# Kernel optimization log

Measured on AMD Instinct MI355X. Metric: run time of the kernel, lower is better.

Reference implementation:

```python
import jax, jax.numpy as jnp
import numpy as np

N_NODES = 100000
N_EDGES = 3200000
IN_C = 256
HID = 32
OUT_C = 64


def setup_inputs() -> dict:
    key = jax.random.key(0)
    ks = jax.random.split(key, 12)
    x = jax.random.normal(ks[0], (N_NODES, IN_C), dtype=jnp.float32)
    edge_index = jax.random.randint(ks[1], (2, N_EDGES), 0, N_NODES, dtype=jnp.int64)

    def lin(kw, kb, fan_in, fan_out):
        bound = 1.0 / np.sqrt(fan_in)
        W = jax.random.uniform(kw, (fan_out, fan_in), jnp.float32, -bound, bound)
        b = jax.random.uniform(kb, (fan_out,), jnp.float32, -bound, bound)
        return W, b

    W0, b0 = lin(ks[2], ks[3], IN_C, HID)
    W1, b1 = lin(ks[4], ks[5], HID, HID)
    W2, b2 = lin(ks[6], ks[7], HID, HID)
    W3, b3 = lin(ks[8], ks[9], HID, HID)
    W4, b4 = lin(ks[10], ks[11], HID, OUT_C)
    return {"x": x, "edge_index": edge_index,
            "W0": W0, "b0": b0, "W1": W1, "b1": b1, "W2": W2, "b2": b2,
            "W3": W3, "b3": b3, "W4": W4, "b4": b4}


def _gcn_norm(edge_index, num_nodes):
    # add self loops, symmetric normalization (PyG gcn_norm, edge_weight = 1)
    loop = jnp.arange(num_nodes, dtype=edge_index.dtype)
    row = jnp.concatenate([edge_index[0], loop])  # source nodes
    col = jnp.concatenate([edge_index[1], loop])  # target nodes
    deg = jax.ops.segment_sum(jnp.ones_like(col, dtype=jnp.float32), col,
                              num_segments=num_nodes)
    dinv = jnp.where(deg > 0, jax.lax.rsqrt(jnp.maximum(deg, 1e-12)), 0.0)
    norm = dinv[row] * dinv[col]
    return row, col, norm


def reference(x, edge_index, W0, b0, W1, b1, W2, b2, W3, b3, W4, b4):
    row, col, norm = _gcn_norm(edge_index, N_NODES)

    def prop(h):
        # gather source features, scale by norm, scatter-add to targets
        return jax.ops.segment_sum(norm[:, None] * h[row], col,
                                   num_segments=N_NODES)

    def sgconv(h, W, b):  # SGConv with K=1: propagate then linear
        return prop(h) @ W.T + b

    h = x @ W0.T + b0
    h = jax.nn.relu(sgconv(h, W1, b1))
    h = jax.nn.relu(sgconv(h, W2, b2))
    h = jax.nn.relu(sgconv(h, W3, b3))
    return h @ W4.T + b4
```

## Files before the change

### kernel.cpp

```cpp
#include <hip/hip_runtime.h>
#include <hip/hip_fp16.h>

#define N_NODES 100000
#define N_EDGES 3200000
#define IN_C 256
#define HID 32
#define OUT_C 64
#define CAP 80
#define NP 100032
#define BINW 256
#define BSH 8
#define NBIN 391
#define BCHUNK 8192

__device__ __forceinline__ float dot4(const float4 a, const float4 b) {
    return a.x * b.x + a.y * b.y + a.z * b.z + a.w * b.w;
}

__device__ __forceinline__ float4 h4tof4(uint2 v) {
    __half2 a = *reinterpret_cast<__half2*>(&v.x);
    __half2 b = *reinterpret_cast<__half2*>(&v.y);
    float2 fa = __half22float2(a), fb = __half22float2(b);
    return make_float4(fa.x, fa.y, fb.x, fb.y);
}
__device__ __forceinline__ uint2 f4toh4(float4 f) {
    __half2 a = __float22half2_rn(make_float2(f.x, f.y));
    __half2 b = __float22half2_rn(make_float2(f.z, f.w));
    uint2 v;
    v.x = *reinterpret_cast<unsigned int*>(&a);
    v.y = *reinterpret_cast<unsigned int*>(&b);
    return v;
}


__global__ __launch_bounds__(256) void k_binhist(const int* __restrict__ col,
                                                 int* __restrict__ binCnt) {
    __shared__ int h[NBIN];
    const int t = threadIdx.x;
    for (int i = t; i < NBIN; i += 256) h[i] = 0;
    __syncthreads();
    const long e0 = (long)blockIdx.x * BCHUNK;
    const long e1 = min((long)N_EDGES, e0 + BCHUNK);
    for (long i = e0 + t; i < e1; i += 256)
        atomicAdd(&h[col[i] >> BSH], 1);
    __syncthreads();
    for (int i = t; i < NBIN; i += 256)
        if (h[i]) atomicAdd(&binCnt[i], h[i]);
}

__global__ void k_binscan(const int* __restrict__ binCnt,
                          int* __restrict__ binStart, int* __restrict__ binCursor) {
    __shared__ int buf[2][512];
    const int t = threadIdx.x;
    int v = (t < NBIN) ? binCnt[t] : 0;
    buf[0][t] = v;
    __syncthreads();
    int s = 0;
    for (int off = 1; off < 512; off <<= 1) {
        int d = s ^ 1;
        int val = buf[s][t];
        if (t >= off) val += buf[s][t - off];
        buf[d][t] = val;
        __syncthreads();
        s = d;
    }
    if (t < NBIN) {
        int st = buf[s][t] - v;
        binStart[t] = st;
        binCursor[t] = st;
    }
}

__global__ __launch_bounds__(256) void k_binscatter(const int* __restrict__ row,
                                                    const int* __restrict__ col,
                                                    int* __restrict__ binCursor,
                                                    int2* __restrict__ pairs) {
    __shared__ int cnt[NBIN];
    __shared__ int ofs[NBIN];
    const int t = threadIdx.x;
    for (int i = t; i < NBIN; i += 256) cnt[i] = 0;
    __syncthreads();
    const long e0 = (long)blockIdx.x * BCHUNK;
    const long e1 = min((long)N_EDGES, e0 + BCHUNK);
    for (long i = e0 + t; i < e1; i += 256)
        atomicAdd(&cnt[col[i] >> BSH], 1);
    __syncthreads();
    for (int i = t; i < NBIN; i += 256) {
        int c = cnt[i];
        ofs[i] = c ? atomicAdd(&binCursor[i], c) : 0;
        cnt[i] = 0;
    }
    __syncthreads();
    for (long i = e0 + t; i < e1; i += 256) {
        int c = col[i];
        int b = c >> BSH;
        int p = ofs[b] + atomicAdd(&cnt[b], 1);
        pairs[p] = make_int2(row[i], c);
    }
}

__global__ __launch_bounds__(256) void k_binbuild(const int2* __restrict__ pairs,
                                                  const int* __restrict__ binStart,
                                                  const int* __restrict__ binCnt,
                                                  int* __restrict__ bucket,
                                                  int* __restrict__ degc,
                                                  float* __restrict__ dinv) {
    __shared__ int cur[BINW];
    const int t = threadIdx.x;
    const int bin = blockIdx.x;
    const int base = bin * BINW;
    cur[t] = 0;
    __syncthreads();
    const int s = binStart[bin], cn = binCnt[bin];
    for (int i = t; i < cn; i += 256) {
        int2 e = pairs[s + i];
        int c = e.y - base;
        int pos = atomicAdd(&cur[c], 1);
        if (pos < CAP) bucket[(size_t)(base + c) * CAP + pos] = e.x;
    }
    __syncthreads();
    int n = base + t;
    if (n < N_NODES) {
        int d = cur[t];
        degc[n] = d;
        dinv[n] = 1.0f / sqrtf((float)(d + 1));
    }
}


__global__ void k_hist(const int* __restrict__ col, int* __restrict__ deg) {
    int i = blockIdx.x * 256 + threadIdx.x;
    if (i < N_EDGES) atomicAdd(&deg[col[i]], 1);
}

__global__ void k_scan1(const int* __restrict__ deg, int* __restrict__ rowptr,
                        int* __restrict__ bsum) {
    __shared__ int buf[2][1024];
    const int t = threadIdx.x, b = blockIdx.x;
    const int i = b * 1024 + t;
    int v = (i < N_NODES) ? deg[i] : 0;
    buf[0][t] = v;
    __syncthreads();
    int src = 0;
    for (int off = 1; off < 1024; off <<= 1) {
        int dst = src ^ 1;
        int val = buf[src][t];
        if (t >= off) val += buf[src][t - off];
        buf[dst][t] = val;
        __syncthreads();
        src = dst;
    }
    int incl = buf[src][t];
    if (i < N_NODES) rowptr[i] = incl - v;
    if (t == 1023) bsum[b] = incl;
}

__global__ void k_scan2(int* __restrict__ bsum, int nb) {
    __shared__ int buf[2][128];
    const int t = threadIdx.x;
    int v = (t < nb) ? bsum[t] : 0;
    buf[0][t] = v;
    __syncthreads();
    int src = 0;
    for (int off = 1; off < 128; off <<= 1) {
        int dst = src ^ 1;
        int val = buf[src][t];
        if (t >= off) val += buf[src][t - off];
        buf[dst][t] = val;
        __syncthreads();
        src = dst;
    }
    if (t < nb) bsum[t] = buf[src][t] - v;
}

__global__ void k_scan3(int* __restrict__ rowptr, const int* __restrict__ bsum) {
    int i = blockIdx.x * 256 + threadIdx.x;
    if (i < N_NODES) rowptr[i] += bsum[i >> 10];
}

__global__ void k_dinv(const int* __restrict__ cnt, int stride,
                       float* __restrict__ dinv, int* __restrict__ degc) {
    int i = blockIdx.x * 256 + threadIdx.x;
    if (i < N_NODES) {
        int d = cnt[i * stride];
        degc[i] = d;
        dinv[i] = 1.0f / sqrtf((float)(d + 1));
    }
}

__global__ void k_scatter(const int* __restrict__ row, const int* __restrict__ col,
                          const int* __restrict__ rowptr, int* __restrict__ cursor,
                          int* __restrict__ csr) {
    int i = blockIdx.x * 256 + threadIdx.x;
    if (i < N_EDGES) {
        int c = col[i];
        int pos = rowptr[c] + atomicAdd(&cursor[c], 1);
        csr[pos] = row[i];
    }
}

__global__ __launch_bounds__(256) void k_lin0(const float4* __restrict__ x4,
                                              const float4* __restrict__ W04,
                                              const float4* __restrict__ b04,
                                              const float* __restrict__ dinv,
                                              uint2* __restrict__ g2) {
    __shared__ float4 Ws[2048];
    const int t = threadIdx.x;
    #pragma unroll
    for (int j = 0; j < 8; ++j) Ws[t + 256 * j] = W04[t + 256 * j];
    __syncthreads();

    const int l = t & 7;
    const int n0 = blockIdx.x * 64 + (t >> 3) * 2;
    if (n0 >= N_NODES) return;
    const bool two = (n0 + 1 < N_NODES);

    float a0[32], a1[32];
    #pragma unroll
    for (int c = 0; c < 32; ++c) { a0[c] = 0.f; a1[c] = 0.f; }

    const float4* xr0 = x4 + (size_t)n0 * 64;
    const float4* xr1 = xr0 + (two ? 64 : 0);
    #pragma unroll
    for (int kk = 0; kk < 8; ++kk) {
        float4 v0 = xr0[kk * 8 + l];
        float4 v1 = xr1[kk * 8 + l];
        #pragma unroll
        for (int c = 0; c < 32; ++c) {
            float4 w = Ws[c * 64 + kk * 8 + l];
            a0[c] += dot4(w, v0);
            a1[c] += dot4(w, v1);
        }
    }
    #pragma unroll
    for (int c = 0; c < 16; ++c) {
        float p0 = a0[c] + __shfl_xor(a0[c], 4, 8);
        float q0 = a0[c + 16] + __shfl_xor(a0[c + 16], 4, 8);
        a0[c] = (l & 4) ? q0 : p0;
        float p1 = a1[c] + __shfl_xor(a1[c], 4, 8);
        float q1 = a1[c + 16] + __shfl_xor(a1[c + 16], 4, 8);
        a1[c] = (l & 4) ? q1 : p1;
    }
    #pragma unroll
    for (int c = 0; c < 8; ++c) {
        float p0 = a0[c] + __shfl_xor(a0[c], 2, 8);
        float q0 = a0[c + 8] + __shfl_xor(a0[c + 8], 2, 8);
        a0[c] = (l & 2) ? q0 : p0;
        float p1 = a1[c] + __shfl_xor(a1[c], 2, 8);
        float q1 = a1[c + 8] + __shfl_xor(a1[c + 8], 2, 8);
        a1[c] = (l & 2) ? q1 : p1;
    }
    #pragma unroll
    for (int c = 0; c < 4; ++c) {
        float p0 = a0[c] + __shfl_xor(a0[c], 1, 8);
        float q0 = a0[c + 4] + __shfl_xor(a0[c + 4], 1, 8);
        a0[c] = (l & 1) ? q0 : p0;
        float p1 = a1[c] + __shfl_xor(a1[c], 1, 8);
        float q1 = a1[c + 4] + __shfl_xor(a1[c + 4], 1, 8);
        a1[c] = (l & 1) ? q1 : p1;
    }
    const float4 bv = b04[l];
    {
        float dv = dinv[n0];
        float4 r = make_float4((a0[0] + bv.x) * dv, (a0[1] + bv.y) * dv,
                               (a0[2] + bv.z) * dv, (a0[3] + bv.w) * dv);
        g2[(size_t)n0 * 8 + l] = f4toh4(r);
    }
    if (two) {
        float dv = dinv[n0 + 1];
        float4 r = make_float4((a1[0] + bv.x) * dv, (a1[1] + bv.y) * dv,
                               (a1[2] + bv.z) * dv, (a1[3] + bv.w) * dv);
        g2[(size_t)(n0 + 1) * 8 + l] = f4toh4(r);
    }
}


__global__ __launch_bounds__(256) void k_prop2(
        const uint2* __restrict__ g2, const int* __restrict__ idx,
        const int* __restrict__ base_arr,
        const int* __restrict__ cnt_arr, int maxcnt,
        const float* __restrict__ dinv,
        const float* __restrict__ W, const float* __restrict__ b,
        uint2* __restrict__ gout2) {
    __shared__ float4 Ws[HID * 9];
    const int t = threadIdx.x;
    { int c = t >> 3, k4 = t & 7; Ws[c * 9 + k4] = ((const float4*)W)[t]; }
    __syncthreads();

    const int l = t & 7;
    const int n = blockIdx.x * 32 + (t >> 3);
    if (n >= N_NODES) return;

    int cnt = cnt_arr[n];
    if (cnt > maxcnt) cnt = maxcnt;
    const int base = base_arr ? base_arr[n] : n * CAP;
    const int* __restrict__ e = idx + base;

    float4 acc = h4tof4(g2[n * 8 + l]);
    int j = 0;
    for (; j + 8 <= cnt; j += 8) {
        int r0 = e[j], r1 = e[j + 1], r2 = e[j + 2], r3 = e[j + 3];
        int r4 = e[j + 4], r5 = e[j + 5], r6 = e[j + 6], r7 = e[j + 7];
        uint2 v0 = g2[r0 * 8 + l], v1 = g2[r1 * 8 + l];
        uint2 v2 = g2[r2 * 8 + l], v3 = g2[r3 * 8 + l];
        uint2 v4 = g2[r4 * 8 + l], v5 = g2[r5 * 8 + l];
        uint2 v6 = g2[r6 * 8 + l], v7 = g2[r7 * 8 + l];
        float4 a0 = h4tof4(v0), a1 = h4tof4(v1), a2 = h4tof4(v2), a3 = h4tof4(v3);
        float4 a4 = h4tof4(v4), a5 = h4tof4(v5), a6 = h4tof4(v6), a7 = h4tof4(v7);
        acc.x += a0.x + a1.x + a2.x + a3.x + a4.x + a5.x + a6.x + a7.x;
        acc.y += a0.y + a1.y + a2.y + a3.y + a4.y + a5.y + a6.y + a7.y;
        acc.z += a0.z + a1.z + a2.z + a3.z + a4.z + a5.z + a6.z + a7.z;
        acc.w += a0.w + a1.w + a2.w + a3.w + a4.w + a5.w + a6.w + a7.w;
    }
    for (; j < cnt; ++j) {
        float4 a = h4tof4(g2[e[j] * 8 + l]);
        acc.x += a.x; acc.y += a.y; acc.z += a.z; acc.w += a.w;
    }

    const float dv = dinv[n];
    float4 y = make_float4(0.f, 0.f, 0.f, 0.f);
    #pragma unroll
    for (int m = 0; m < 8; ++m) {
        float4 sv;
        sv.x = __shfl(acc.x, m, 8);
        sv.y = __shfl(acc.y, m, 8);
        sv.z = __shfl(acc.z, m, 8);
        sv.w = __shfl(acc.w, m, 8);
        y.x += dot4(Ws[(4 * l + 0) * 9 + m], sv);
        y.y += dot4(Ws[(4 * l + 1) * 9 + m], sv);
        y.z += dot4(Ws[(4 * l + 2) * 9 + m], sv);
        y.w += dot4(Ws[(4 * l + 3) * 9 + m], sv);
    }
    const float4 bb = ((const float4*)b)[l];
    y.x = fmaxf(bb.x + dv * y.x, 0.f) * dv;
    y.y = fmaxf(bb.y + dv * y.y, 0.f) * dv;
    y.z = fmaxf(bb.z + dv * y.z, 0.f) * dv;
    y.w = fmaxf(bb.w + dv * y.w, 0.f) * dv;
    gout2[n * 8 + l] = f4toh4(y);
}

__global__ __launch_bounds__(256) void k_last2(
        const uint2* __restrict__ g2, const int* __restrict__ idx,
        const int* __restrict__ base_arr,
        const int* __restrict__ cnt_arr, int maxcnt,
        const float* __restrict__ dinv,
        const float* __restrict__ W3, const float* __restrict__ b3,
        const float* __restrict__ W4, const float* __restrict__ b4,
        float4* __restrict__ out4) {
    __shared__ float4 W3s[HID * 9];
    __shared__ float4 W4s[OUT_C * 9];
    const int t = threadIdx.x;
    { int c = t >> 3, k4 = t & 7; W3s[c * 9 + k4] = ((const float4*)W3)[t]; }
    #pragma unroll
    for (int f = t; f < 512; f += 256) {
        int c = f >> 3, k4 = f & 7;
        W4s[c * 9 + k4] = ((const float4*)W4)[f];
    }
    __syncthreads();

    const int l = t & 7;
    const int n = blockIdx.x * 32 + (t >> 3);
    if (n >= N_NODES) return;

    int cnt = cnt_arr[n];
    if (cnt > maxcnt) cnt = maxcnt;
    const int base = base_arr ? base_arr[n] : n * CAP;
    const int* __restrict__ e = idx + base;

    float4 acc = h4tof4(g2[n * 8 + l]);
    int j = 0;
    for (; j + 8 <= cnt; j += 8) {
        int r0 = e[j], r1 = e[j + 1], r2 = e[j + 2], r3 = e[j + 3];
        int r4 = e[j + 4], r5 = e[j + 5], r6 = e[j + 6], r7 = e[j + 7];
        uint2 v0 = g2[r0 * 8 + l], v1 = g2[r1 * 8 + l];
        uint2 v2 = g2[r2 * 8 + l], v3 = g2[r3 * 8 + l];
        uint2 v4 = g2[r4 * 8 + l], v5 = g2[r5 * 8 + l];
        uint2 v6 = g2[r6 * 8 + l], v7 = g2[r7 * 8 + l];
        float4 a0 = h4tof4(v0), a1 = h4tof4(v1), a2 = h4tof4(v2), a3 = h4tof4(v3);
        float4 a4 = h4tof4(v4), a5 = h4tof4(v5), a6 = h4tof4(v6), a7 = h4tof4(v7);
        acc.x += a0.x + a1.x + a2.x + a3.x + a4.x + a5.x + a6.x + a7.x;
        acc.y += a0.y + a1.y + a2.y + a3.y + a4.y + a5.y + a6.y + a7.y;
        acc.z += a0.z + a1.z + a2.z + a3.z + a4.z + a5.z + a6.z + a7.z;
        acc.w += a0.w + a1.w + a2.w + a3.w + a4.w + a5.w + a6.w + a7.w;
    }
    for (; j < cnt; ++j) {
        float4 a = h4tof4(g2[e[j] * 8 + l]);
        acc.x += a.x; acc.y += a.y; acc.z += a.z; acc.w += a.w;
    }

    const float dv = dinv[n];
    float4 y = make_float4(0.f, 0.f, 0.f, 0.f);
    #pragma unroll
    for (int m = 0; m < 8; ++m) {
        float4 sv;
        sv.x = __shfl(acc.x, m, 8);
        sv.y = __shfl(acc.y, m, 8);
        sv.z = __shfl(acc.z, m, 8);
        sv.w = __shfl(acc.w, m, 8);
        y.x += dot4(W3s[(4 * l + 0) * 9 + m], sv);
        y.y += dot4(W3s[(4 * l + 1) * 9 + m], sv);
        y.z += dot4(W3s[(4 * l + 2) * 9 + m], sv);
        y.w += dot4(W3s[(4 * l + 3) * 9 + m], sv);
    }
    const float4 b3v = ((const float4*)b3)[l];
    float4 h;
    h.x = fmaxf(b3v.x + dv * y.x, 0.f);
    h.y = fmaxf(b3v.y + dv * y.y, 0.f);
    h.z = fmaxf(b3v.z + dv * y.z, 0.f);
    h.w = fmaxf(b3v.w + dv * y.w, 0.f);

    float4 ya = make_float4(0.f, 0.f, 0.f, 0.f);
    float4 yb = make_float4(0.f, 0.f, 0.f, 0.f);
    #pragma unroll
    for (int m = 0; m < 8; ++m) {
        float4 hv;
        hv.x = __shfl(h.x, m, 8);
        hv.y = __shfl(h.y, m, 8);
        hv.z = __shfl(h.z, m, 8);
        hv.w = __shfl(h.w, m, 8);
        ya.x += dot4(W4s[(4 * l + 0) * 9 + m], hv);
        ya.y += dot4(W4s[(4 * l + 1) * 9 + m], hv);
        ya.z += dot4(W4s[(4 * l + 2) * 9 + m], hv);
        ya.w += dot4(W4s[(4 * l + 3) * 9 + m], hv);
        yb.x += dot4(W4s[(32 + 4 * l + 0) * 9 + m], hv);
        yb.y += dot4(W4s[(32 + 4 * l + 1) * 9 + m], hv);
        yb.z += dot4(W4s[(32 + 4 * l + 2) * 9 + m], hv);
        yb.w += dot4(W4s[(32 + 4 * l + 3) * 9 + m], hv);
    }
    const float4 b4a = ((const float4*)b4)[l];
    const float4 b4b = ((const float4*)b4)[8 + l];
    ya.x += b4a.x; ya.y += b4a.y; ya.z += b4a.z; ya.w += b4a.w;
    yb.x += b4b.x; yb.y += b4b.y; yb.z += b4b.z; yb.w += b4b.w;
    out4[n * 16 + l] = ya;
    out4[n * 16 + 8 + l] = yb;
}


extern "C" void kernel_launch(void* const* d_in, const int* in_sizes, int n_in,
                              void* d_out, int out_size, void* d_ws, size_t ws_size,
                              hipStream_t stream) {
    const float* x   = (const float*)d_in[0];
    const int*   ei  = (const int*)d_in[1];
    const int*   row = ei;
    const int*   col = ei + N_EDGES;
    const float* W0 = (const float*)d_in[2];
    const float* b0 = (const float*)d_in[3];
    const float* W1 = (const float*)d_in[4];
    const float* b1 = (const float*)d_in[5];
    const float* W2 = (const float*)d_in[6];
    const float* b2 = (const float*)d_in[7];
    const float* W3 = (const float*)d_in[8];
    const float* b3 = (const float*)d_in[9];
    const float* W4 = (const float*)d_in[10];
    const float* b4 = (const float*)d_in[11];
    float* out = (float*)d_out;

    const int EB = (N_EDGES + 255) / 256;
    const int NB256 = (N_NODES + 255) / 256;
    const int NB1024 = (N_NODES + 1023) / 1024;
    const int CB = (N_EDGES + BCHUNK - 1) / BCHUNK;
    const int LB = (N_NODES + 63) / 64;
    const int PB2 = (N_NODES + 31) / 32;

    const size_t UNION_BYTES = (size_t)N_EDGES * sizeof(int2);
    const size_t FAST_BYTES =
        (size_t)N_NODES * CAP * 4 + 2ull * NP * 4 + 3ull * 512 * 4 + UNION_BYTES;

    if (ws_size >= FAST_BYTES) {
        int*   bucket    = (int*)d_ws;
        float* dinv      = (float*)(bucket + (size_t)N_NODES * CAP);
        int*   degc      = (int*)(dinv + NP);
        int*   binCnt    = degc + NP;
        int*   binStart  = binCnt + 512;
        int*   binCursor = binStart + 512;
        char*  uni       = (char*)(binCursor + 512);
        int2*  pairs     = (int2*)uni;
        uint2* gA        = (uint2*)uni;
        uint2* gB        = gA + (size_t)N_NODES * 8;

        hipMemsetAsync(binCnt, 0, 512 * sizeof(int), stream);
        k_binhist<<<CB, 256, 0, stream>>>(col, binCnt);
        k_binscan<<<1, 512, 0, stream>>>(binCnt, binStart, binCursor);
        k_binscatter<<<CB, 256, 0, stream>>>(row, col, binCursor, pairs);
        k_binbuild<<<NBIN, 256, 0, stream>>>(pairs, binStart, binCnt,
                                             bucket, degc, dinv);

        k_lin0<<<LB, 256, 0, stream>>>((const float4*)x, (const float4*)W0,
                                       (const float4*)b0, dinv, gA);

        k_prop2<<<PB2, 256, 0, stream>>>(gA, bucket, nullptr, degc, CAP,
                                         dinv, W1, b1, gB);
        k_prop2<<<PB2, 256, 0, stream>>>(gB, bucket, nullptr, degc, CAP,
                                         dinv, W2, b2, gA);
        k_last2<<<PB2, 256, 0, stream>>>(gA, bucket, nullptr, degc, CAP,
                                         dinv, W3, b3, W4, b4, (float4*)out);
    } else {
        int*   deg    = (int*)d_ws;
        int*   rowptr = deg + NP;
        int*   cursor = rowptr + NP;
        int*   bsum   = cursor + NP;
        float* dinv   = (float*)(bsum + 128);
        int*   csr    = (int*)(dinv + NP);
        uint2* gA     = (uint2*)(csr + N_EDGES);
        uint2* gB     = gA + (size_t)N_NODES * 8;

        hipMemsetAsync(deg, 0, (size_t)NP * 3 * sizeof(int), stream);
        k_hist<<<EB, 256, 0, stream>>>(col, deg);
        k_scan1<<<NB1024, 1024, 0, stream>>>(deg, rowptr, bsum);
        k_scan2<<<1, 128, 0, stream>>>(bsum, NB1024);
        k_scan3<<<NB256, 256, 0, stream>>>(rowptr, bsum);
        k_dinv<<<NB256, 256, 0, stream>>>(deg, 1, dinv, cursor);
        hipMemsetAsync(cursor, 0, (size_t)NP * sizeof(int), stream);
        k_scatter<<<EB, 256, 0, stream>>>(row, col, rowptr, cursor, csr);

        k_lin0<<<LB, 256, 0, stream>>>((const float4*)x, (const float4*)W0,
                                       (const float4*)b0, dinv, gA);

        k_prop2<<<PB2, 256, 0, stream>>>(gA, csr, rowptr, deg, 1 << 30,
                                         dinv, W1, b1, gB);
        k_prop2<<<PB2, 256, 0, stream>>>(gB, csr, rowptr, deg, 1 << 30,
                                         dinv, W2, b2, gA);
        k_last2<<<PB2, 256, 0, stream>>>(gA, csr, rowptr, deg, 1 << 30,
                                         dinv, W3, b3, W4, b4, (float4*)out);
    }
}
```

Baseline: 516.4 us.

## Compute first linear layer with split-fp16 MFMA instead of scalar FP32 dot products

Replaces the scalar FP32 x@W0^T kernel with one that uses 16x16x32 f16 MFMA instructions. Each operand is split into a high and low fp16 part (three MFMAs per tile) to keep roughly FP32 accuracy, and W0 is prescaled by 16 to avoid fp16 underflow. The goal is to move the ~100000x256x32 GEMM off the VALU so it is bound by the 100 MB read of x. The cost is extra conversion work and a small accuracy risk from the split-precision scheme.

```diff
diff --git a/kernel.cpp b/kernel.cpp
--- a/kernel.cpp
+++ b/kernel.cpp
@@ -13,6 +13,9 @@
 #define NBIN 391
 #define BCHUNK 8192
 
+typedef _Float16 f16x8 __attribute__((ext_vector_type(8)));
+typedef float f32x4 __attribute__((ext_vector_type(4)));
+
 __device__ __forceinline__ float dot4(const float4 a, const float4 b) {
     return a.x * b.x + a.y * b.y + a.z * b.z + a.w * b.w;
 }
@@ -199,78 +202,102 @@
     }
 }
 
-__global__ __launch_bounds__(256) void k_lin0(const float4* __restrict__ x4,
-                                              const float4* __restrict__ W04,
-                                              const float4* __restrict__ b04,
-                                              const float* __restrict__ dinv,
-                                              uint2* __restrict__ g2) {
-    __shared__ float4 Ws[2048];
-    const int t = threadIdx.x;
-    #pragma unroll
-    for (int j = 0; j < 8; ++j) Ws[t + 256 * j] = W04[t + 256 * j];
-    __syncthreads();
-
-    const int l = t & 7;
-    const int n0 = blockIdx.x * 64 + (t >> 3) * 2;
-    if (n0 >= N_NODES) return;
-    const bool two = (n0 + 1 < N_NODES);
-
-    float a0[32], a1[32];
-    #pragma unroll
-    for (int c = 0; c < 32; ++c) { a0[c] = 0.f; a1[c] = 0.f; }
-
-    const float4* xr0 = x4 + (size_t)n0 * 64;
-    const float4* xr1 = xr0 + (two ? 64 : 0);
-    #pragma unroll
-    for (int kk = 0; kk < 8; ++kk) {
-        float4 v0 = xr0[kk * 8 + l];
-        float4 v1 = xr1[kk * 8 + l];
+__global__ __launch_bounds__(256) void k_lin0_mfma(
+        const float* __restrict__ x,
+        const float* __restrict__ W0,
+        const float* __restrict__ b0,
+        const float* __restrict__ dinv,
+        uint2* __restrict__ g2) {
+    __shared__ f16x8 WH[1024];
+    __shared__ f16x8 WL[1024];
+
+    const int t = threadIdx.x;
+    const int w = t >> 6;
+    const int l = t & 63;
+    const int lr = l & 15;
+    const int lg = l >> 4;
+
+    for (int s = t; s < 1024; s += 256) {
+        const int lane = s & 63;
+        const int mtks = s >> 6;
+        const int ks = mtks & 7, mt = mtks >> 3;
+        const float* wr = W0 + (size_t)(mt * 16 + (lane & 15)) * IN_C
+                             + ks * 32 + (lane >> 4) * 8;
+        float4 a0 = *(const float4*)(wr);
+        float4 a1 = *(const float4*)(wr + 4);
+        float v[8] = {a0.x, a0.y, a0.z, a0.w, a1.x, a1.y, a1.z, a1.w};
+        f16x8 h, lo;
         #pragma unroll
-        for (int c = 0; c < 32; ++c) {
-            float4 w = Ws[c * 64 + kk * 8 + l];
-            a0[c] += dot4(w, v0);
-            a1[c] += dot4(w, v1);
+        for (int e = 0; e < 8; ++e) {
+            float sv = v[e] * 16.0f;
+            _Float16 hh = (_Float16)sv;
+            h[e] = hh;
+            lo[e] = (_Float16)(sv - (float)hh);
         }
-    }
-    #pragma unroll
-    for (int c = 0; c < 16; ++c) {
-        float p0 = a0[c] + __shfl_xor(a0[c], 4, 8);
-        float q0 = a0[c + 16] + __shfl_xor(a0[c + 16], 4, 8);
-        a0[c] = (l & 4) ? q0 : p0;
-        float p1 = a1[c] + __shfl_xor(a1[c], 4, 8);
-        float q1 = a1[c + 16] + __shfl_xor(a1[c + 16], 4, 8);
-        a1[c] = (l & 4) ? q1 : p1;
-    }
-    #pragma unroll
-    for (int c = 0; c < 8; ++c) {
-        float p0 = a0[c] + __shfl_xor(a0[c], 2, 8);
-        float q0 = a0[c + 8] + __shfl_xor(a0[c + 8], 2, 8);
-        a0[c] = (l & 2) ? q0 : p0;
-        float p1 = a1[c] + __shfl_xor(a1[c], 2, 8);
-        float q1 = a1[c + 8] + __shfl_xor(a1[c + 8], 2, 8);
-        a1[c] = (l & 2) ? q1 : p1;
-    }
-    #pragma unroll
-    for (int c = 0; c < 4; ++c) {
-        float p0 = a0[c] + __shfl_xor(a0[c], 1, 8);
-        float q0 = a0[c + 4] + __shfl_xor(a0[c + 4], 1, 8);
-        a0[c] = (l & 1) ? q0 : p0;
-        float p1 = a1[c] + __shfl_xor(a1[c], 1, 8);
-        float q1 = a1[c + 4] + __shfl_xor(a1[c + 4], 1, 8);
-        a1[c] = (l & 1) ? q1 : p1;
-    }
-    const float4 bv = b04[l];
-    {
-        float dv = dinv[n0];
-        float4 r = make_float4((a0[0] + bv.x) * dv, (a0[1] + bv.y) * dv,
-                               (a0[2] + bv.z) * dv, (a0[3] + bv.w) * dv);
-        g2[(size_t)n0 * 8 + l] = f4toh4(r);
-    }
-    if (two) {
-        float dv = dinv[n0 + 1];
-        float4 r = make_float4((a1[0] + bv.x) * dv, (a1[1] + bv.y) * dv,
-                               (a1[2] + bv.z) * dv, (a1[3] + bv.w) * dv);
-        g2[(size_t)(n0 + 1) * 8 + l] = f4toh4(r);
+        WH[s] = h;
+        WL[s] = lo;
+    }
+    __syncthreads();
+
+    const int unit = blockIdx.x * 4 + w;
+    if (unit * 32 >= N_NODES) return;
+    const int n0 = unit * 32;
+
+    f32x4 acc[2][2];
+    #pragma unroll
+    for (int mt = 0; mt < 2; ++mt)
+        #pragma unroll
+        for (int nt = 0; nt < 2; ++nt)
+            acc[mt][nt] = (f32x4){0.f, 0.f, 0.f, 0.f};
+
+    const float* xr0 = x + (size_t)(n0 + lr) * IN_C + lg * 8;
+    const float* xr1 = x + (size_t)(n0 + 16 + lr) * IN_C + lg * 8;
+
+    #pragma unroll
+    for (int ks = 0; ks < 8; ++ks) {
+        float4 u0 = *(const float4*)(xr0 + ks * 32);
+        float4 u1 = *(const float4*)(xr0 + ks * 32 + 4);
+        float4 v0 = *(const float4*)(xr1 + ks * 32);
+        float4 v1 = *(const float4*)(xr1 + ks * 32 + 4);
+        float fu[8] = {u0.x, u0.y, u0.z, u0.w, u1.x, u1.y, u1.z, u1.w};
+        float fv[8] = {v0.x, v0.y, v0.z, v0.w, v1.x, v1.y, v1.z, v1.w};
+        f16x8 xh0, xl0, xh1, xl1;
+        #pragma unroll
+        for (int e = 0; e < 8; ++e) {
+            _Float16 h0 = (_Float16)fu[e];
+            xh0[e] = h0;
+            xl0[e] = (_Float16)(fu[e] - (float)h0);
+            _Float16 h1 = (_Float16)fv[e];
+            xh1[e] = h1;
+            xl1[e] = (_Float16)(fv[e] - (float)h1);
+        }
+        #pragma unroll
+        for (int mt = 0; mt < 2; ++mt) {
+            f16x8 wh = WH[mt * 512 + ks * 64 + l];
+            f16x8 wl = WL[mt * 512 + ks * 64 + l];
+            acc[mt][0] = __builtin_amdgcn_mfma_f32_16x16x32_f16(wh, xh0, acc[mt][0], 0, 0, 0);
+            acc[mt][0] = __builtin_amdgcn_mfma_f32_16x16x32_f16(wh, xl0, acc[mt][0], 0, 0, 0);
+            acc[mt][0] = __builtin_amdgcn_mfma_f32_16x16x32_f16(wl, xh0, acc[mt][0], 0, 0, 0);
+            acc[mt][1] = __builtin_amdgcn_mfma_f32_16x16x32_f16(wh, xh1, acc[mt][1], 0, 0, 0);
+            acc[mt][1] = __builtin_amdgcn_mfma_f32_16x16x32_f16(wh, xl1, acc[mt][1], 0, 0, 0);
+            acc[mt][1] = __builtin_amdgcn_mfma_f32_16x16x32_f16(wl, xh1, acc[mt][1], 0, 0, 0);
+        }
+    }
+
+    #pragma unroll
+    for (int nt = 0; nt < 2; ++nt) {
+        const int node = n0 + nt * 16 + lr;
+        const float dv = dinv[node];
+        #pragma unroll
+        for (int mt = 0; mt < 2; ++mt) {
+            const float4 bb = *(const float4*)(b0 + mt * 16 + lg * 4);
+            f32x4 a = acc[mt][nt];
+            float4 r = make_float4((a[0] * 0.0625f + bb.x) * dv,
+                                   (a[1] * 0.0625f + bb.y) * dv,
+                                   (a[2] * 0.0625f + bb.z) * dv,
+                                   (a[3] * 0.0625f + bb.w) * dv);
+            g2[(size_t)node * 8 + mt * 4 + lg] = f4toh4(r);
+        }
     }
 }
 
@@ -459,7 +486,8 @@
     const int NB256 = (N_NODES + 255) / 256;
     const int NB1024 = (N_NODES + 1023) / 1024;
     const int CB = (N_EDGES + BCHUNK - 1) / BCHUNK;
-    const int LB = (N_NODES + 63) / 64;
+    const int UNITS = (N_NODES + 31) / 32;
+    const int LB0 = (UNITS + 3) / 4;
     const int PB2 = (N_NODES + 31) / 32;
 
     const size_t UNION_BYTES = (size_t)N_EDGES * sizeof(int2);
@@ -485,8 +513,7 @@
         k_binbuild<<<NBIN, 256, 0, stream>>>(pairs, binStart, binCnt,
                                              bucket, degc, dinv);
 
-        k_lin0<<<LB, 256, 0, stream>>>((const float4*)x, (const float4*)W0,
-                                       (const float4*)b0, dinv, gA);
+        k_lin0_mfma<<<LB0, 256, 0, stream>>>(x, W0, b0, dinv, gA);
 
         k_prop2<<<PB2, 256, 0, stream>>>(gA, bucket, nullptr, degc, CAP,
                                          dinv, W1, b1, gB);
@@ -513,8 +540,7 @@
         hipMemsetAsync(cursor, 0, (size_t)NP * sizeof(int), stream);
         k_scatter<<<EB, 256, 0, stream>>>(row, col, rowptr, cursor, csr);
 
-        k_lin0<<<LB, 256, 0, stream>>>((const float4*)x, (const float4*)W0,
-                                       (const float4*)b0, dinv, gA);
+        k_lin0_mfma<<<LB0, 256, 0, stream>>>(x, W0, b0, dinv, gA);
 
         k_prop2<<<PB2, 256, 0, stream>>>(gA, csr, rowptr, deg, 1 << 30,
                                          dinv, W1, b1, gB);
```

After: 465.9 us. -9.8%, faster.
